# Kernel optimization log

Hardware: AMD Instinct MI355X
Metric: run time of the kernel (lower is better)

## Reference

```python
import jax, jax.numpy as jnp
import numpy as np

D_MODEL = 512
NUM_HEADS = 8


def setup_inputs() -> dict:
    key = jax.random.key(0)
    ks = jax.random.split(key, 6)
    B, S, D = 4, 2048, D_MODEL
    Q = jax.random.normal(ks[0], (B, S, D), dtype=jnp.float32)
    K = jax.random.normal(ks[1], (B, S, D), dtype=jnp.float32)
    V = jax.random.normal(ks[2], (B, S, D), dtype=jnp.float32)
    # boolean mask, True = masked out; random so no row is fully masked
    mask = jax.random.randint(ks[3], (B, S, S), 0, 2).astype(jnp.bool_)
    scale = 1.0 / np.sqrt(D)
    Wq = jax.random.normal(ks[4], (D, D), dtype=jnp.float32) * scale
    Wo = jax.random.normal(ks[5], (D, D), dtype=jnp.float32) * scale
    return {"Q": Q, "K": K, "V": V, "mask": mask, "Wq": Wq, "Wo": Wo}


def reference(Q, K, V, mask, Wq, Wo):
    B, S, D = Q.shape
    H = NUM_HEADS
    dk = D // H
    # Faithful to the source: Q_Linear's weight (Wq) is applied to Q, K AND V
    # (K_Linear / V_Linear are dead parameters in the original module).
    q = (Q @ Wq.T).reshape(B, S, H, dk)
    k = (K @ Wq.T).reshape(B, S, H, dk)
    v = (V @ Wq.T).reshape(B, S, H, dk)
    # scores: [B, H, Sq, Sk]
    scores = jnp.einsum("bqhd,bkhd->bhqk", q, k)
    scores = jnp.where(mask[:, None, :, :], -jnp.inf, scores)
    w = jax.nn.softmax(scores / jnp.sqrt(jnp.asarray(dk, scores.dtype)), axis=-1)
    c = jnp.einsum("bhqk,bkhd->bqhd", w, v).reshape(B, S, D)
    return c @ Wo.T
```

## Files before the change

### kernel.cpp

```cpp
#include <hip/hip_runtime.h>
#include <math.h>

#define B_ 4
#define S_ 2048
#define D_ 512
#define H_ 8
#define DK_ 64
#define MROWS (B_ * S_)

typedef short bf16x8 __attribute__((ext_vector_type(8)));
typedef float f32x4 __attribute__((ext_vector_type(4)));
typedef float f32x16 __attribute__((ext_vector_type(16)));

static __device__ __forceinline__ unsigned short f2bf(float x) {
    unsigned int u = __float_as_uint(x);
    return (unsigned short)((u + 0x7FFFu + ((u >> 16) & 1u)) >> 16);
}
static __device__ __forceinline__ unsigned int cvt_pk_bf16(float a, float b) {
    unsigned int r;
    asm("v_cvt_pk_bf16_f32 %0, %1, %2" : "=v"(r) : "v"(a), "v"(b));
    return r;
}
static __device__ __forceinline__ float exp2_fast(float x) {
    float r;
    asm("v_exp_f32 %0, %1" : "=v"(r) : "v"(x));
    return r;
}
static __device__ __forceinline__ void gld_lds16(const unsigned short* g, unsigned short* l) {
    __builtin_amdgcn_global_load_lds(
        (const __attribute__((address_space(1))) unsigned int*)g,
        (__attribute__((address_space(3))) unsigned int*)l, 16, 0, 0);
}
static __device__ __forceinline__ void plswap(unsigned int& a, unsigned int& b) {
    asm volatile("v_permlane32_swap_b32 %0, %1" : "+v"(a), "+v"(b));
}

#define NXE (MROWS * D_)
#define NWE (D_ * D_)
#define CAST_BLOCKS ((3 * NXE + 2 * NWE) / 8 / 256)
#define MASKE (B_ * S_ * S_)
#define MASK_BLOCKS (MASKE / 256 / 4)
#define MASKB_BYTE (MASKE / 256 / 16)

__global__ __launch_bounds__(256) void prep(const float* __restrict__ Q,
                                            const float* __restrict__ K,
                                            const float* __restrict__ V,
                                            const float* __restrict__ Wq,
                                            const float* __restrict__ Wo,
                                            const void* __restrict__ mask,
                                            unsigned short* __restrict__ Qb,
                                            unsigned short* __restrict__ Kb,
                                            unsigned short* __restrict__ Vb,
                                            unsigned short* __restrict__ Wqb,
                                            unsigned short* __restrict__ Wob,
                                            unsigned long long* __restrict__ mb) {
    if (blockIdx.x < CAST_BLOCKS) {
        const int NA = NXE / 8;
        const int NWn = NWE / 8;
        int id = blockIdx.x * 256 + threadIdx.x;
        const float* src;
        unsigned short* dst;
        if (id < 3 * NA) {
            int a = id / NA, r = id - a * NA;
            src = (a == 0 ? Q : a == 1 ? K : V) + (size_t)r * 8;
            dst = (a == 0 ? Qb : a == 1 ? Kb : Vb) + (size_t)r * 8;
        } else {
            int r = id - 3 * NA;
            int a = r / NWn; r -= a * NWn;
            src = (a == 0 ? Wq : Wo) + (size_t)r * 8;
            dst = (a == 0 ? Wqb : Wob) + (size_t)r * 8;
        }
        float4 x = *(const float4*)src;
        float4 y = *(const float4*)(src + 4);
        unsigned short u[8] = {f2bf(x.x), f2bf(x.y), f2bf(x.z), f2bf(x.w),
                               f2bf(y.x), f2bf(y.y), f2bf(y.z), f2bf(y.w)};
        *(uint4*)dst = *(const uint4*)u;
    } else {
        const int mblk = blockIdx.x - CAST_BLOCKS;
        unsigned int accw = 0;
        if ((threadIdx.x & 63) == 0) {
            const unsigned int* mw0 = (const unsigned int*)mask;
            #pragma unroll
            for (int i = 0; i < 16; ++i) accw |= mw0[i];
        }
        accw = __shfl(accw, 0);
        const bool bytemode = (accw & 0xFFFFFF00u) != 0u;
        if (bytemode) {
            if (mblk >= MASKB_BYTE) return;
            const int gid = mblk * 256 + threadIdx.x;
            uint4 x = ((const uint4*)mask)[gid];
            unsigned int n[4];
            const unsigned int xs[4] = {x.x, x.y, x.z, x.w};
            #pragma unroll
            for (int i = 0; i < 4; ++i) {
                unsigned int y = xs[i];
                y |= y >> 4; y |= y >> 2; y |= y >> 1;
                y &= 0x01010101u;
                n[i] = (y * 0x01020408u) >> 24;
            }
            const unsigned short piece =
                (unsigned short)(n[0] | (n[1] << 4) | (n[2] << 8) | (n[3] << 12));
            ((unsigned short*)mb)[gid] = piece;
        } else {
            const int wid = (mblk * 256 + threadIdx.x) >> 6;
            const int lane = threadIdx.x & 63;
            const unsigned int* mi = (const unsigned int*)mask;
            const size_t base = (size_t)wid * 256;
            unsigned long long b0 = __ballot(mi[base + lane] != 0);
            unsigned long long b1 = __ballot(mi[base + 64 + lane] != 0);
            unsigned long long b2 = __ballot(mi[base + 128 + lane] != 0);
            unsigned long long b3 = __ballot(mi[base + 192 + lane] != 0);
            if (lane == 0) {
                const size_t wix = base >> 6;
                mb[wix] = b0; mb[wix + 1] = b1; mb[wix + 2] = b2; mb[wix + 3] = b3;
            }
        }
    }
}

__global__ __launch_bounds__(256) void proj3(const unsigned short* __restrict__ Qb,
                                             const unsigned short* __restrict__ Kb,
                                             const unsigned short* __restrict__ Vb,
                                             const unsigned short* __restrict__ Wqb,
                                             unsigned short* __restrict__ qs,
                                             unsigned short* __restrict__ kbo,
                                             unsigned short* __restrict__ vt) {
    __shared__ unsigned short smx[24576];
    const int t = threadIdx.x;
    const int w = t >> 6, lane = t & 63, col = lane & 15, quad = lane >> 4;
    const int bm = blockIdx.x * 128, bn = blockIdx.y * 128;
    const int z = blockIdx.z;
    const unsigned short* X = (z == 0) ? Qb : (z == 1) ? Kb : Vb;
    const int wm = (w >> 1) * 64, wn = (w & 1) * 64;

    const int sr = w * 32 + (lane >> 2);
    const int ssw = (((lane & 3) ^ ((lane >> 3) & 3)) * 8);
    const unsigned short* ags = X + (size_t)(bm + sr) * D_ + ssw;
    const unsigned short* bgs = Wqb + (size_t)(bn + sr) * D_ + ssw;
    const int pseg = ((quad ^ ((col >> 1) & 3)) * 8);

    f32x4 acc[4][4];
    #pragma unroll
    for (int i = 0; i < 4; ++i)
        #pragma unroll
        for (int j = 0; j < 4; ++j) acc[i][j] = (f32x4){0.f, 0.f, 0.f, 0.f};

    #pragma unroll
    for (int s = 0; s < 2; ++s) {
        const int bb = s * 8192;
        gld_lds16(ags + s * 32, &smx[bb + w * 1024]);
        gld_lds16(ags + 16 * D_ + s * 32, &smx[bb + w * 1024 + 512]);
        gld_lds16(bgs + s * 32, &smx[bb + 4096 + w * 1024]);
        gld_lds16(bgs + 16 * D_ + s * 32, &smx[bb + 4096 + w * 1024 + 512]);
    }
    __asm__ __volatile__("s_waitcnt vmcnt(4)" ::: "memory");
    __builtin_amdgcn_s_barrier();

    #pragma unroll 1
    for (int ts = 0; ts < 16; ++ts) {
        if (ts + 2 < 16) {
            const int nb = ((ts + 2) % 3) * 8192;
            const int ko = (ts + 2) * 32;
            gld_lds16(ags + ko, &smx[nb + w * 1024]);
            gld_lds16(ags + 16 * D_ + ko, &smx[nb + w * 1024 + 512]);
            gld_lds16(bgs + ko, &smx[nb + 4096 + w * 1024]);
            gld_lds16(bgs + 16 * D_ + ko, &smx[nb + 4096 + w * 1024 + 512]);
        }
        __builtin_amdgcn_sched_barrier(0);

        const int cb = (ts % 3) * 8192;
        bf16x8 af[4], bg[4];
        #pragma unroll
        for (int i = 0; i < 4; ++i)
            af[i] = *(const bf16x8*)&smx[cb + (wm + i * 16 + col) * 32 + pseg];
        #pragma unroll
        for (int j = 0; j < 4; ++j)
            bg[j] = *(const bf16x8*)&smx[cb + 4096 + (wn + j * 16 + col) * 32 + pseg];
        #pragma unroll
        for (int i = 0; i < 4; ++i)
            #pragma unroll
            for (int j = 0; j < 4; ++j)
                acc[i][j] = __builtin_amdgcn_mfma_f32_16x16x32_bf16(
                    af[i], bg[j], acc[i][j], 0, 0, 0);

        if (ts < 14) {
            __asm__ __volatile__("s_waitcnt vmcnt(4)" ::: "memory");
        } else if (ts == 14) {
            __asm__ __volatile__("s_waitcnt vmcnt(0)" ::: "memory");
        }
        if (ts < 15) __builtin_amdgcn_s_barrier();
    }

    if (z == 2) {
        #pragma unroll
        for (int i = 0; i < 4; ++i) {
            const int R = bm + wm + i * 16 + quad * 4;
            const int bb = R >> 11, s0 = R & (S_ - 1);
            #pragma unroll
            for (int j = 0; j < 4; ++j) {
                const int C = bn + wn + j * 16 + col;
                const int hh = C >> 6, dd = C & (DK_ - 1);
                ushort4 u = make_ushort4(f2bf(acc[i][j][0]), f2bf(acc[i][j][1]),
                                         f2bf(acc[i][j][2]), f2bf(acc[i][j][3]));
                *(ushort4*)&vt[(((size_t)bb * H_ + hh) * DK_ + dd) * S_ + s0] = u;
            }
        }
    } else {
        unsigned short* O = (z == 0) ? qs : kbo;
        const float scl = (z == 0) ? 0.18033688f : 1.0f;
        #pragma unroll
        for (int i = 0; i < 4; ++i)
            #pragma unroll
            for (int j = 0; j < 4; ++j) {
                const int R = bm + wm + i * 16 + quad * 4;
                const int C = bn + wn + j * 16 + col;
                #pragma unroll
                for (int r = 0; r < 4; ++r)
                    O[(size_t)(R + r) * D_ + C] = f2bf(acc[i][j][r] * scl);
            }
    }
}

__global__ __launch_bounds__(256) void gemm_out(const unsigned short* __restrict__ o0,
                                                const unsigned short* __restrict__ o1,
                                                const float* __restrict__ l0,
                                                const float* __restrict__ l1,
                                                const unsigned short* __restrict__ Wob,
                                                float* __restrict__ Out) {
    __shared__ unsigned short smx[20480];
    __shared__ float invt[128 * 8];
    const int t = threadIdx.x;
    const int w = t >> 6, lane = t & 63, col = lane & 15, quad = lane >> 4;
    const int bm = blockIdx.x * 128, bn = blockIdx.y * 128;
    const int wm = (w >> 1) * 64, wn = (w & 1) * 64;

    const int sr = w * 32 + (lane >> 2);
    const int ssw = (((lane & 3) ^ ((lane >> 3) & 3)) * 8);
    const unsigned short* ag0 = o0 + (size_t)(bm + sr) * D_ + ssw;
    const unsigned short* ag1 = o1 + (size_t)(bm + sr) * D_ + ssw;
    const unsigned short* bgs = Wob + (size_t)(bn + sr) * D_ + ssw;
    const int pseg = ((quad ^ ((col >> 1) & 3)) * 8);

    f32x4 acc[4][4];
    #pragma unroll
    for (int i = 0; i < 4; ++i)
        #pragma unroll
        for (int j = 0; j < 4; ++j) acc[i][j] = (f32x4){0.f, 0.f, 0.f, 0.f};

    gld_lds16(bgs, &smx[8192 + w * 1024]);
    gld_lds16(bgs + 16 * D_, &smx[8192 + w * 1024 + 512]);
    uint4 p00 = *(const uint4*)(ag0);
    uint4 p01 = *(const uint4*)(ag1);
    uint4 p10 = *(const uint4*)(ag0 + 16 * D_);
    uint4 p11 = *(const uint4*)(ag1 + 16 * D_);
    gld_lds16(bgs + 32, &smx[12288 + w * 1024]);
    gld_lds16(bgs + 16 * D_ + 32, &smx[12288 + w * 1024 + 512]);

    #pragma unroll
    for (int i = 0; i < 4; ++i) {
        const int e = t * 4 + i;
        const int row = bm + (e >> 3), hh = e & 7;
        invt[e] = 1.0f / (l0[(size_t)row * H_ + hh] + l1[(size_t)row * H_ + hh]);
    }
    __asm__ __volatile__("s_waitcnt lgkmcnt(0)" ::: "memory");
    __builtin_amdgcn_s_barrier();

    {
        const float ivA = invt[sr * 8];
        const float ivB = invt[(sr + 16) * 8];
        const unsigned short* pa = (const unsigned short*)&p00;
        const unsigned short* pb = (const unsigned short*)&p01;
        unsigned short ob[8];
        #pragma unroll
        for (int i = 0; i < 8; ++i) {
            float fa = __uint_as_float((unsigned int)pa[i] << 16);
            float fb = __uint_as_float((unsigned int)pb[i] << 16);
            ob[i] = f2bf((fa + fb) * ivA);
        }
        *(uint4*)&smx[w * 1024 + lane * 8] = *(const uint4*)ob;
        pa = (const unsigned short*)&p10;
        pb = (const unsigned short*)&p11;
        #pragma unroll
        for (int i = 0; i < 8; ++i) {
            float fa = __uint_as_float((unsigned int)pa[i] << 16);
            float fb = __uint_as_float((unsigned int)pb[i] << 16);
            ob[i] = f2bf((fa + fb) * ivB);
        }
        *(uint4*)&smx[w * 1024 + 512 + lane * 8] = *(const uint4*)ob;
    }
    __asm__ __volatile__("s_waitcnt lgkmcnt(0)" ::: "memory");
    __builtin_amdgcn_s_barrier();

    #pragma unroll 1
    for (int ts = 0; ts < 16; ++ts) {
        uint4 a00, a01, a10, a11;
        const bool hasA = (ts + 1 < 16);
        if (hasA) {
            const int ko = (ts + 1) * 32;
            a00 = *(const uint4*)(ag0 + ko);
            a01 = *(const uint4*)(ag1 + ko);
            a10 = *(const uint4*)(ag0 + 16 * D_ + ko);
            a11 = *(const uint4*)(ag1 + 16 * D_ + ko);
        }
        if (ts + 2 < 16) {
            const int bb = 8192 + ((ts + 2) % 3) * 4096;
            const int ko = (ts + 2) * 32;
            gld_lds16(bgs + ko, &smx[bb + w * 1024]);
            gld_lds16(bgs + 16 * D_ + ko, &smx[bb + w * 1024 + 512]);
        }
        __builtin_amdgcn_sched_barrier(0);

        const int ab = (ts & 1) * 4096;
        const int bb = 8192 + (ts % 3) * 4096;
        bf16x8 af[4], bg[4];
        #pragma unroll
        for (int i = 0; i < 4; ++i)
            af[i] = *(const bf16x8*)&smx[ab + (wm + i * 16 + col) * 32 + pseg];
        #pragma unroll
        for (int j = 0; j < 4; ++j)
            bg[j] = *(const bf16x8*)&smx[bb + (wn + j * 16 + col) * 32 + pseg];
        #pragma unroll
        for (int i = 0; i < 4; ++i)
            #pragma unroll
            for (int j = 0; j < 4; ++j)
                acc[i][j] = __builtin_amdgcn_mfma_f32_16x16x32_bf16(
                    af[i], bg[j], acc[i][j], 0, 0, 0);

        if (hasA) {
            const int hh = (ts + 1) >> 1;
            const float ivA = invt[sr * 8 + hh];
            const float ivB = invt[(sr + 16) * 8 + hh];
            const int na = ((ts + 1) & 1) * 4096;
            const unsigned short* pa = (const unsigned short*)&a00;
            const unsigned short* pb = (const unsigned short*)&a01;
            unsigned short ob[8];
            #pragma unroll
            for (int i = 0; i < 8; ++i) {
                float fa = __uint_as_float((unsigned int)pa[i] << 16);
                float fb = __uint_as_float((unsigned int)pb[i] << 16);
                ob[i] = f2bf((fa + fb) * ivA);
            }
            *(uint4*)&smx[na + w * 1024 + lane * 8] = *(const uint4*)ob;
            pa = (const unsigned short*)&a10;
            pb = (const unsigned short*)&a11;
            #pragma unroll
            for (int i = 0; i < 8; ++i) {
                float fa = __uint_as_float((unsigned int)pa[i] << 16);
                float fb = __uint_as_float((unsigned int)pb[i] << 16);
                ob[i] = f2bf((fa + fb) * ivB);
            }
            *(uint4*)&smx[na + w * 1024 + 512 + lane * 8] = *(const uint4*)ob;
        }
        __asm__ __volatile__("s_waitcnt lgkmcnt(0)" ::: "memory");
        if (ts < 15) __builtin_amdgcn_s_barrier();
    }

    #pragma unroll
    for (int i = 0; i < 4; ++i)
        #pragma unroll
        for (int j = 0; j < 4; ++j) {
            const int R = bm + wm + i * 16 + quad * 4;
            const int C = bn + wn + j * 16 + col;
            #pragma unroll
            for (int r = 0; r < 4; ++r)
                Out[(size_t)(R + r) * D_ + C] = acc[i][j][r];
        }
}

__global__ __launch_bounds__(256, 4) void attn_mfma(
        const unsigned short* __restrict__ qb,
        const unsigned short* __restrict__ kb,
        const unsigned short* __restrict__ vt,
        const unsigned long long* __restrict__ mb,
        unsigned short* __restrict__ o0,
        unsigned short* __restrict__ o1,
        float* __restrict__ l0,
        float* __restrict__ l1) {
    __shared__ unsigned short sm[16384];
    const int t = threadIdx.x;
    const int w = t >> 6;
    const int lane = t & 63;
    const int q5 = lane & 31;
    const int hi = lane >> 5;
    const int h = blockIdx.y;
    const int b = blockIdx.z >> 1;
    const int khalf = blockIdx.z & 1;
    const int bh = b * H_ + h;
    const int qrow0 = blockIdx.x * 128 + w * 32;

    unsigned short* opart = khalf ? o1 : o0;
    float* lpart = khalf ? l1 : l0;

    const unsigned int chk = cvt_pk_bf16(1.0f, 2.0f);
    const bool ablow = ((chk & 0xFFFFu) == 0x3F80u);

    bf16x8 qf[4];
    {
        const unsigned short* qp =
            qb + (size_t)(b * S_ + qrow0 + q5) * D_ + h * DK_ + hi * 8;
        #pragma unroll
        for (int dsl = 0; dsl < 4; ++dsl)
            qf[dsl] = *(const bf16x8*)(qp + dsl * 16);
    }

    bf16x8 ones8;
    #pragma unroll
    for (int i = 0; i < 8; ++i) ones8[i] = (short)0x3F80;

    const float CREF = 8.656170245f;
    f32x16 Oa, Ob, lacc, crefv;
    #pragma unroll
    for (int i = 0; i < 16; ++i) {
        Oa[i] = 0.f; Ob[i] = 0.f; lacc[i] = 0.f; crefv[i] = -CREF;
    }

    const int kbeg = khalf * (S_ / 2);

    const int ln8 = lane >> 3;
    const int fs8 = ((lane & 7) ^ ln8) * 8;
    const int r0 = w * 16 + ln8;
    const unsigned short* pK0 = kb + (size_t)(b * S_ + kbeg + r0) * D_ + h * DK_ + fs8;
    const unsigned short* pK1 = pK0 + 8 * D_;
    const unsigned short* pV0 = vt + ((size_t)bh * DK_ + r0) * S_ + kbeg + fs8;
    const unsigned short* pV1 = pV0 + 8 * S_;

    const unsigned long long* mbase =
        mb + (size_t)(b * S_ + qrow0 + q5) * (S_ / 64) + (kbeg >> 6);

    gld_lds16(pK0, &sm[w * 1024]);
    gld_lds16(pK1, &sm[w * 1024 + 512]);
    gld_lds16(pV0, &sm[4096 + w * 1024]);
    gld_lds16(pV1, &sm[4096 + w * 1024 + 512]);
    pK0 += 64 * D_; pK1 += 64 * D_; pV0 += 64; pV1 += 64;

    const int x7 = (q5 & 7);

    #pragma unroll 1
    for (int ti = 0; ti < 16; ++ti) {
        unsigned long long mw = mbase[ti];
        __builtin_amdgcn_sched_barrier(0);
        if (ti < 15) {
            const int nb = (ti & 1) ? 0 : 8192;
            gld_lds16(pK0, &sm[nb + w * 1024]);
            gld_lds16(pK1, &sm[nb + w * 1024 + 512]);
            gld_lds16(pV0, &sm[nb + 4096 + w * 1024]);
            gld_lds16(pV1, &sm[nb + 4096 + w * 1024 + 512]);
            pK0 += 64 * D_; pK1 += 64 * D_; pV0 += 64; pV1 += 64;
            __asm__ __volatile__("s_waitcnt vmcnt(5)" ::: "memory");
        } else {
            __asm__ __volatile__("s_waitcnt vmcnt(1)" ::: "memory");
        }
        __builtin_amdgcn_s_barrier();

        const int KB = (ti & 1) ? 8192 : 0;
        const int VB = KB + 4096;
        const unsigned long long msh = mw >> (hi * 4);

        #pragma unroll
        for (int kbi = 0; kbi < 2; ++kbi) {
            const int krow = KB + (kbi * 32 + q5) * 64;
            __builtin_amdgcn_s_setprio(1);
            bf16x8 kf0 = *(const bf16x8*)&sm[krow + ((hi) ^ x7) * 8];
            f32x16 S = __builtin_amdgcn_mfma_f32_32x32x16_bf16(kf0, qf[0], crefv, 0, 0, 0);
            #pragma unroll
            for (int dsl = 1; dsl < 4; ++dsl) {
                bf16x8 kf = *(const bf16x8*)&sm[krow + (((dsl << 1) | hi) ^ x7) * 8];
                S = __builtin_amdgcn_mfma_f32_32x32x16_bf16(kf, qf[dsl], S, 0, 0, 0);
            }
            __builtin_amdgcn_s_setprio(0);

            float p[16];
            #pragma unroll
            for (int r = 0; r < 16; ++r) {
                const int c = kbi * 32 + (r & 3) + 8 * (r >> 2);
                const bool msk = ((msh >> c) & 1ull) != 0ull;
                p[r] = exp2_fast(msk ? -1e30f : S[r]);
            }

            #pragma unroll
            for (int ksl = 0; ksl < 2; ++ksl) {
                const int bsl = ksl * 8;
                unsigned int uA = ablow ? cvt_pk_bf16(p[bsl], p[bsl + 1])
                                        : cvt_pk_bf16(p[bsl + 1], p[bsl]);
                unsigned int uB = ablow ? cvt_pk_bf16(p[bsl + 2], p[bsl + 3])
                                        : cvt_pk_bf16(p[bsl + 3], p[bsl + 2]);
                unsigned int uC = ablow ? cvt_pk_bf16(p[bsl + 4], p[bsl + 5])
                                        : cvt_pk_bf16(p[bsl + 5], p[bsl + 4]);
                unsigned int uD = ablow ? cvt_pk_bf16(p[bsl + 6], p[bsl + 7])
                                        : cvt_pk_bf16(p[bsl + 7], p[bsl + 6]);
                plswap(uA, uC);
                plswap(uB, uD);
                union { unsigned int u[4]; bf16x8 v; } pa;
                pa.u[0] = uA; pa.u[1] = uB; pa.u[2] = uC; pa.u[3] = uD;

                const int slice = kbi * 2 + ksl;
                const int vseg = (((slice << 1) | hi) ^ x7) * 8;
                bf16x8 vf0 = *(const bf16x8*)&sm[VB + q5 * 64 + vseg];
                bf16x8 vf1 = *(const bf16x8*)&sm[VB + (32 + q5) * 64 + vseg];
                __builtin_amdgcn_s_setprio(1);
                lacc = __builtin_amdgcn_mfma_f32_32x32x16_bf16(pa.v, ones8, lacc, 0, 0, 0);
                Oa = __builtin_amdgcn_mfma_f32_32x32x16_bf16(pa.v, vf0, Oa, 0, 0, 0);
                Ob = __builtin_amdgcn_mfma_f32_32x32x16_bf16(pa.v, vf1, Ob, 0, 0, 0);
                __builtin_amdgcn_s_setprio(0);
            }
        }

        __builtin_amdgcn_s_barrier();
    }

    #pragma unroll
    for (int r = 0; r < 16; ++r) {
        const int qq = (r & 3) + 8 * (r >> 2) + 4 * hi;
        const size_t row = (size_t)(b * S_ + qrow0 + qq);
        opart[row * D_ + h * DK_ + q5]      = f2bf(Oa[r]);
        opart[row * D_ + h * DK_ + 32 + q5] = f2bf(Ob[r]);
        if (q5 == 0) lpart[row * H_ + h] = lacc[r];
    }
}

extern "C" void kernel_launch(void* const* d_in, const int* in_sizes, int n_in,
                              void* d_out, int out_size, void* d_ws, size_t ws_size,
                              hipStream_t stream) {
    const float* Q    = (const float*)d_in[0];
    const float* K    = (const float*)d_in[1];
    const float* V    = (const float*)d_in[2];
    const void*  mask = d_in[3];
    const float* Wq   = (const float*)d_in[4];
    const float* Wo   = (const float*)d_in[5];
    float* out = (float*)d_out;

    const size_t NX = (size_t)MROWS * D_;
    const size_t NW = (size_t)D_ * D_;
    unsigned short* Qb   = (unsigned short*)d_ws;
    unsigned short* Kb   = Qb + NX;
    unsigned short* Vb   = Kb + NX;
    unsigned short* Wqb  = Vb + NX;
    unsigned short* Wob  = Wqb + NW;
    unsigned short* qbuf = Wob + NW;
    unsigned short* kbuf = qbuf + NX;
    unsigned short* vtb  = kbuf + NX;
    unsigned short* cbuf = vtb + NX;
    unsigned long long* mb = (unsigned long long*)(cbuf + NX);

    unsigned short* o0 = Qb;
    unsigned short* o1 = Kb;
    float* l0 = (float*)Vb;
    float* l1 = l0 + (size_t)MROWS * H_;

    prep<<<dim3(CAST_BLOCKS + MASK_BLOCKS), dim3(256), 0, stream>>>(
        Q, K, V, Wq, Wo, mask, Qb, Kb, Vb, Wqb, Wob, mb);

    proj3<<<dim3(MROWS / 128, D_ / 128, 3), dim3(256), 0, stream>>>(
        Qb, Kb, Vb, Wqb, qbuf, kbuf, vtb);

    attn_mfma<<<dim3(S_ / 128, H_, B_ * 2), dim3(256), 0, stream>>>(
        qbuf, kbuf, vtb, mb, o0, o1, l0, l1);

    gemm_out<<<dim3(MROWS / 128, D_ / 128), dim3(256), 0, stream>>>(
        o0, o1, l0, l1, Wob, out);
}
```

Baseline: 246.4 us.

## Split attention key range four ways when workspace allows, merging partials in output GEMM

The attention kernel now takes a runtime split count and key length, so the key dimension can be divided into four partitions instead of two. Each partition writes its own unnormalized output and row-sum buffers, and the output projection kernel sums four partials when enabled. The aim is more workgroups for the 16x8x4 attention grid, giving better occupancy across the GPU's compute units. The cost is extra partial-output traffic and extra loads in the output GEMM, and the four-way path depends on the workspace being large enough.

Result: slower. 258.2 us (+4.8%).

```diff
diff --git a/kernel.cpp b/kernel.cpp
--- a/kernel.cpp
+++ b/kernel.cpp
@@ -15,6 +15,9 @@
 static __device__ __forceinline__ unsigned short f2bf(float x) {
     unsigned int u = __float_as_uint(x);
     return (unsigned short)((u + 0x7FFFu + ((u >> 16) & 1u)) >> 16);
+}
+static __device__ __forceinline__ float bf2f(unsigned short u) {
+    return __uint_as_float((unsigned int)u << 16);
 }
 static __device__ __forceinline__ unsigned int cvt_pk_bf16(float a, float b) {
     unsigned int r;
@@ -223,10 +226,15 @@
 
 __global__ __launch_bounds__(256) void gemm_out(const unsigned short* __restrict__ o0,
                                                 const unsigned short* __restrict__ o1,
+                                                const unsigned short* __restrict__ o2,
+                                                const unsigned short* __restrict__ o3,
                                                 const float* __restrict__ l0,
                                                 const float* __restrict__ l1,
+                                                const float* __restrict__ l2,
+                                                const float* __restrict__ l3,
                                                 const unsigned short* __restrict__ Wob,
-                                                float* __restrict__ Out) {
+                                                float* __restrict__ Out,
+                                                const int np4) {
     __shared__ unsigned short smx[20480];
     __shared__ float invt[128 * 8];
     const int t = threadIdx.x;
@@ -236,8 +244,11 @@
 
     const int sr = w * 32 + (lane >> 2);
     const int ssw = (((lane & 3) ^ ((lane >> 3) & 3)) * 8);
-    const unsigned short* ag0 = o0 + (size_t)(bm + sr) * D_ + ssw;
-    const unsigned short* ag1 = o1 + (size_t)(bm + sr) * D_ + ssw;
+    const size_t aoff = (size_t)(bm + sr) * D_ + ssw;
+    const unsigned short* ag0 = o0 + aoff;
+    const unsigned short* ag1 = o1 + aoff;
+    const unsigned short* ag2 = o2 + aoff;
+    const unsigned short* ag3 = o3 + aoff;
     const unsigned short* bgs = Wob + (size_t)(bn + sr) * D_ + ssw;
     const int pseg = ((quad ^ ((col >> 1) & 3)) * 8);
 
@@ -251,8 +262,11 @@
     gld_lds16(bgs + 16 * D_, &smx[8192 + w * 1024 + 512]);
     uint4 p00 = *(const uint4*)(ag0);
     uint4 p01 = *(const uint4*)(ag1);
+    uint4 p02, p03, p12, p13;
+    if (np4) { p02 = *(const uint4*)(ag2); p03 = *(const uint4*)(ag3); }
     uint4 p10 = *(const uint4*)(ag0 + 16 * D_);
     uint4 p11 = *(const uint4*)(ag1 + 16 * D_);
+    if (np4) { p12 = *(const uint4*)(ag2 + 16 * D_); p13 = *(const uint4*)(ag3 + 16 * D_); }
     gld_lds16(bgs + 32, &smx[12288 + w * 1024]);
     gld_lds16(bgs + 16 * D_ + 32, &smx[12288 + w * 1024 + 512]);
 
@@ -260,7 +274,9 @@
     for (int i = 0; i < 4; ++i) {
         const int e = t * 4 + i;
         const int row = bm + (e >> 3), hh = e & 7;
-        invt[e] = 1.0f / (l0[(size_t)row * H_ + hh] + l1[(size_t)row * H_ + hh]);
+        float s = l0[(size_t)row * H_ + hh] + l1[(size_t)row * H_ + hh];
+        if (np4) s += l2[(size_t)row * H_ + hh] + l3[(size_t)row * H_ + hh];
+        invt[e] = 1.0f / s;
     }
     __asm__ __volatile__("s_waitcnt lgkmcnt(0)" ::: "memory");
     __builtin_amdgcn_s_barrier();
@@ -270,21 +286,25 @@
         const float ivB = invt[(sr + 16) * 8];
         const unsigned short* pa = (const unsigned short*)&p00;
         const unsigned short* pb = (const unsigned short*)&p01;
+        const unsigned short* pc = (const unsigned short*)&p02;
+        const unsigned short* pd = (const unsigned short*)&p03;
         unsigned short ob[8];
         #pragma unroll
         for (int i = 0; i < 8; ++i) {
-            float fa = __uint_as_float((unsigned int)pa[i] << 16);
-            float fb = __uint_as_float((unsigned int)pb[i] << 16);
-            ob[i] = f2bf((fa + fb) * ivA);
+            float fa = bf2f(pa[i]) + bf2f(pb[i]);
+            if (np4) fa += bf2f(pc[i]) + bf2f(pd[i]);
+            ob[i] = f2bf(fa * ivA);
         }
         *(uint4*)&smx[w * 1024 + lane * 8] = *(const uint4*)ob;
         pa = (const unsigned short*)&p10;
         pb = (const unsigned short*)&p11;
+        pc = (const unsigned short*)&p12;
+        pd = (const unsigned short*)&p13;
         #pragma unroll
         for (int i = 0; i < 8; ++i) {
-            float fa = __uint_as_float((unsigned int)pa[i] << 16);
-            float fb = __uint_as_float((unsigned int)pb[i] << 16);
-            ob[i] = f2bf((fa + fb) * ivB);
+            float fa = bf2f(pa[i]) + bf2f(pb[i]);
+            if (np4) fa += bf2f(pc[i]) + bf2f(pd[i]);
+            ob[i] = f2bf(fa * ivB);
         }
         *(uint4*)&smx[w * 1024 + 512 + lane * 8] = *(const uint4*)ob;
     }
@@ -293,14 +313,16 @@
 
     #pragma unroll 1
     for (int ts = 0; ts < 16; ++ts) {
-        uint4 a00, a01, a10, a11;
+        uint4 a00, a01, a02, a03, a10, a11, a12, a13;
         const bool hasA = (ts + 1 < 16);
         if (hasA) {
             const int ko = (ts + 1) * 32;
             a00 = *(const uint4*)(ag0 + ko);
             a01 = *(const uint4*)(ag1 + ko);
+            if (np4) { a02 = *(const uint4*)(ag2 + ko); a03 = *(const uint4*)(ag3 + ko); }
             a10 = *(const uint4*)(ag0 + 16 * D_ + ko);
             a11 = *(const uint4*)(ag1 + 16 * D_ + ko);
+            if (np4) { a12 = *(const uint4*)(ag2 + 16 * D_ + ko); a13 = *(const uint4*)(ag3 + 16 * D_ + ko); }
         }
         if (ts + 2 < 16) {
             const int bb = 8192 + ((ts + 2) % 3) * 4096;
@@ -333,21 +355,25 @@
             const int na = ((ts + 1) & 1) * 4096;
             const unsigned short* pa = (const unsigned short*)&a00;
             const unsigned short* pb = (const unsigned short*)&a01;
+            const unsigned short* pc = (const unsigned short*)&a02;
+            const unsigned short* pd = (const unsigned short*)&a03;
             unsigned short ob[8];
             #pragma unroll
             for (int i = 0; i < 8; ++i) {
-                float fa = __uint_as_float((unsigned int)pa[i] << 16);
-                float fb = __uint_as_float((unsigned int)pb[i] << 16);
-                ob[i] = f2bf((fa + fb) * ivA);
+                float fa = bf2f(pa[i]) + bf2f(pb[i]);
+                if (np4) fa += bf2f(pc[i]) + bf2f(pd[i]);
+                ob[i] = f2bf(fa * ivA);
             }
             *(uint4*)&smx[na + w * 1024 + lane * 8] = *(const uint4*)ob;
             pa = (const unsigned short*)&a10;
             pb = (const unsigned short*)&a11;
+            pc = (const unsigned short*)&a12;
+            pd = (const unsigned short*)&a13;
             #pragma unroll
             for (int i = 0; i < 8; ++i) {
-                float fa = __uint_as_float((unsigned int)pa[i] << 16);
-                float fb = __uint_as_float((unsigned int)pb[i] << 16);
-                ob[i] = f2bf((fa + fb) * ivB);
+                float fa = bf2f(pa[i]) + bf2f(pb[i]);
+                if (np4) fa += bf2f(pc[i]) + bf2f(pd[i]);
+                ob[i] = f2bf(fa * ivB);
             }
             *(uint4*)&smx[na + w * 1024 + 512 + lane * 8] = *(const uint4*)ob;
         }
@@ -374,8 +400,13 @@
         const unsigned long long* __restrict__ mb,
         unsigned short* __restrict__ o0,
         unsigned short* __restrict__ o1,
+        unsigned short* __restrict__ o2,
+        unsigned short* __restrict__ o3,
         float* __restrict__ l0,
-        float* __restrict__ l1) {
+        float* __restrict__ l1,
+        float* __restrict__ l2,
+        float* __restrict__ l3,
+        const int nspl, const int klen) {
     __shared__ unsigned short sm[16384];
     const int t = threadIdx.x;
     const int w = t >> 6;
@@ -383,13 +414,14 @@
     const int q5 = lane & 31;
     const int hi = lane >> 5;
     const int h = blockIdx.y;
-    const int b = blockIdx.z >> 1;
-    const int khalf = blockIdx.z & 1;
+    const int kq = blockIdx.z % nspl;
+    const int b = blockIdx.z / nspl;
     const int bh = b * H_ + h;
     const int qrow0 = blockIdx.x * 128 + w * 32;
-
-    unsigned short* opart = khalf ? o1 : o0;
-    float* lpart = khalf ? l1 : l0;
+    const int NT = klen >> 6;
+
+    unsigned short* opart = (kq == 0) ? o0 : (kq == 1) ? o1 : (kq == 2) ? o2 : o3;
+    float* lpart = (kq == 0) ? l0 : (kq == 1) ? l1 : (kq == 2) ? l2 : l3;
 
     const unsigned int chk = cvt_pk_bf16(1.0f, 2.0f);
     const bool ablow = ((chk & 0xFFFFu) == 0x3F80u);
@@ -414,7 +446,7 @@
         Oa[i] = 0.f; Ob[i] = 0.f; lacc[i] = 0.f; crefv[i] = -CREF;
     }
 
-    const int kbeg = khalf * (S_ / 2);
+    const int kbeg = kq * klen;
 
     const int ln8 = lane >> 3;
     const int fs8 = ((lane & 7) ^ ln8) * 8;
@@ -436,10 +468,10 @@
     const int x7 = (q5 & 7);
 
     #pragma unroll 1
-    for (int ti = 0; ti < 16; ++ti) {
+    for (int ti = 0; ti < NT; ++ti) {
         unsigned long long mw = mbase[ti];
         __builtin_amdgcn_sched_barrier(0);
-        if (ti < 15) {
+        if (ti < NT - 1) {
             const int nb = (ti & 1) ? 0 : 8192;
             gld_lds16(pK0, &sm[nb + w * 1024]);
             gld_lds16(pK1, &sm[nb + w * 1024 + 512]);
@@ -544,8 +576,15 @@
 
     unsigned short* o0 = Qb;
     unsigned short* o1 = Kb;
+    unsigned short* o2 = cbuf;
+    unsigned short* o3 = (unsigned short*)(mb + MASKE / 64);
     float* l0 = (float*)Vb;
     float* l1 = l0 + (size_t)MROWS * H_;
+    float* l2 = l0 + 2 * (size_t)MROWS * H_;
+    float* l3 = l0 + 3 * (size_t)MROWS * H_;
+
+    const size_t need4 = (size_t)((char*)(o3 + NX) - (char*)d_ws);
+    const int nspl = (ws_size >= need4) ? 4 : 2;
 
     prep<<<dim3(CAST_BLOCKS + MASK_BLOCKS), dim3(256), 0, stream>>>(
         Q, K, V, Wq, Wo, mask, Qb, Kb, Vb, Wqb, Wob, mb);
@@ -553,9 +592,9 @@
     proj3<<<dim3(MROWS / 128, D_ / 128, 3), dim3(256), 0, stream>>>(
         Qb, Kb, Vb, Wqb, qbuf, kbuf, vtb);
 
-    attn_mfma<<<dim3(S_ / 128, H_, B_ * 2), dim3(256), 0, stream>>>(
-        qbuf, kbuf, vtb, mb, o0, o1, l0, l1);
+    attn_mfma<<<dim3(S_ / 128, H_, B_ * nspl), dim3(256), 0, stream>>>(
+        qbuf, kbuf, vtb, mb, o0, o1, o2, o3, l0, l1, l2, l3, nspl, S_ / nspl);
 
     gemm_out<<<dim3(MROWS / 128, D_ / 128), dim3(256), 0, stream>>>(
-        o0, o1, l0, l1, Wob, out);
-}
+        o0, o1, o2, o3, l0, l1, l2, l3, Wob, out, nspl == 4 ? 1 : 0);
+}
```
